# Performance work log

Measured on AMD Instinct MI355X. Metric: run time of the kernel, lower is better.

The kernel has to match this reference:

```python
import jax, jax.numpy as jnp
import numpy as np
from jax import lax

B = 1024          # batch
R = 100           # number of radical heads (TOP_RADICALS)


def _conv(x, w, b, padding):
    y = lax.conv_general_dilated(
        x, w, window_strides=(1, 1), padding=padding,
        dimension_numbers=('NCHW', 'OIHW', 'NCHW'))
    return y + b[None, :, None, None]


def _maxpool2(x):
    return lax.reduce_window(x, -jnp.inf, lax.max,
                             (1, 1, 2, 2), (1, 1, 2, 2), 'VALID')


def setup_inputs() -> dict:
    key = jax.random.key(0)
    ks = jax.random.split(key, 20)
    s = 0.05
    inp = {
        'x': jax.random.normal(ks[0], (B, 1, 98, 98), jnp.float32),
        'conv1_w': jax.random.normal(ks[1], (6, 1, 3, 3), jnp.float32) * s,
        'conv1_b': jnp.zeros((6,), jnp.float32),
        'conv2_w': jax.random.normal(ks[2], (4, 6, 6, 6), jnp.float32) * s,
        'conv2_b': jnp.zeros((4,), jnp.float32),
        'conv3_w': jax.random.normal(ks[3], (2, 4, 3, 3), jnp.float32) * s,
        'conv3_b': jnp.zeros((2,), jnp.float32),
        'fc1_w': jax.random.normal(ks[4], (200, 400), jnp.float32) * s,
        'fc1_b': jnp.zeros((400,), jnp.float32),
        'fc2_w': jax.random.normal(ks[5], (400, 200), jnp.float32) * s,
        'fc2_b': jnp.zeros((200,), jnp.float32),
        # all R per-radical heads stacked: Linear(200,140)->(140,84)->(84,42)->(42,4)
        'h1_w': jax.random.normal(ks[6], (R, 200, 140), jnp.float32) * s,
        'h1_b': jnp.zeros((R, 140), jnp.float32),
        'h2_w': jax.random.normal(ks[7], (R, 140, 84), jnp.float32) * s,
        'h2_b': jnp.zeros((R, 84), jnp.float32),
        'h3_w': jax.random.normal(ks[8], (R, 84, 42), jnp.float32) * s,
        'h3_b': jnp.zeros((R, 42), jnp.float32),
        'h4_w': jax.random.normal(ks[9], (R, 42, 4), jnp.float32) * s,
        'h4_b': jnp.zeros((R, 4), jnp.float32),
    }
    return inp


def reference(x, conv1_w, conv1_b, conv2_w, conv2_b, conv3_w, conv3_b,
              fc1_w, fc1_b, fc2_w, fc2_b,
              h1_w, h1_b, h2_w, h2_b, h3_w, h3_b, h4_w, h4_b):
    # conv trunk: conv -> relu -> maxpool, x3
    x = _maxpool2(jax.nn.relu(_conv(x, conv1_w, conv1_b, [(1, 1), (1, 1)])))  # [B,6,49,49]
    x = _maxpool2(jax.nn.relu(_conv(x, conv2_w, conv2_b, 'VALID')))           # [B,4,22,22]
    x = _maxpool2(jax.nn.relu(_conv(x, conv3_w, conv3_b, 'VALID')))           # [B,2,10,10]
    x = x.reshape(x.shape[0], -1)                                             # [B,200]
    # shared MLP trunk
    x = jax.nn.relu(x @ fc1_w + fc1_b)   # [B,400]
    x = jax.nn.relu(x @ fc2_w + fc2_b)   # [B,200]
    # R independent 4-layer heads, fused into batched einsums
    h = jax.nn.relu(jnp.einsum('bd,rdh->brh', x, h1_w) + h1_b)  # [B,R,140]
    h = jax.nn.relu(jnp.einsum('brd,rdh->brh', h, h2_w) + h2_b)  # [B,R,84]
    h = jax.nn.relu(jnp.einsum('brd,rdh->brh', h, h3_w) + h3_b)  # [B,R,42]
    h = jnp.einsum('brd,rdh->brh', h, h4_w) + h4_b               # [B,R,4]
    # torch.cat over heads along dim=1 == reshape [B, R*4]
    return h.reshape(h.shape[0], -1)
```

## Files before the change

### kernel.cpp

```cpp
#include <hip/hip_runtime.h>

#define NB 1024
#define NR 100

typedef _Float16 half_t;
typedef half_t f16x8 __attribute__((ext_vector_type(8)));
typedef float f32x4 __attribute__((ext_vector_type(4)));
typedef float f32x2 __attribute__((ext_vector_type(2)));

__device__ __forceinline__ int kmap2(int g, int j) {
    return g*4 + (j & 3) + ((j >> 2) << 4);
}

__device__ __forceinline__ f32x2 pkfma(f32x2 a, float s, f32x2 c) {
    return __builtin_elementwise_fma(a, (f32x2){s, s}, c);
}

#define GLDS(gsrc, ldst) \
    __builtin_amdgcn_global_load_lds( \
        (const __attribute__((address_space(1))) void*)(gsrc), \
        (__attribute__((address_space(3))) void*)(ldst), 16, 0, 0)

#define EOFF 2268
__global__ __launch_bounds__(256, 5) void conv12_k(const float* __restrict__ x,
        const float* __restrict__ wp1, const float* __restrict__ b1c,
        const float* __restrict__ wp2, const float* __restrict__ b2c,
        float* __restrict__ out) {
    __shared__ float img[56*56];
    __shared__ float c1p[4374];
    const int blk = blockIdx.x;
    const int b  = blk >> 2;
    const int qy = (blk >> 1) & 1, qx = blk & 1;
    const int R0 = 44*qy - 1, C0 = 44*qx - 1;
    const int tid = threadIdx.x;
    const float* xb = x + (size_t)b * 9604;

    for (int i = tid; i < 56*56; i += 256) {
        const int rr = i / 56, cc = i - rr*56;
        const int gr = R0 + rr, gc = C0 + cc;
        float v = 0.f;
        if (gr >= 0 && gr < 98 && gc >= 0 && gc < 98) v = xb[gr*98 + gc];
        img[i] = v;
    }
    __syncthreads();

    for (int pos = tid; pos < 729; pos += 256) {
        const int py = pos / 27, px = pos - py*27;
        float p[4][4];
        const float* base = img + (2*py)*56 + 2*px;
        #pragma unroll
        for (int u = 0; u < 4; ++u) {
            *(f32x2*)&p[u][0] = *(const f32x2*)(base + u*56);
            *(f32x2*)&p[u][2] = *(const f32x2*)(base + u*56 + 2);
        }
        f32x2 a2[3][4];
        #pragma unroll
        for (int g = 0; g < 3; ++g) {
            const f32x2 bv = *(const f32x2*)(b1c + g*2);
            a2[g][0] = a2[g][1] = a2[g][2] = a2[g][3] = bv;
        }
        #pragma unroll
        for (int ky = 0; ky < 3; ++ky)
            #pragma unroll
            for (int kx = 0; kx < 3; ++kx) {
                const int k = ky*3 + kx;
                const float q0 = p[ky  ][kx], q1 = p[ky  ][kx+1];
                const float q2 = p[ky+1][kx], q3 = p[ky+1][kx+1];
                #pragma unroll
                for (int g = 0; g < 3; ++g) {
                    const f32x2 wv = *(const f32x2*)(wp1 + (k*3+g)*2);
                    a2[g][0] = pkfma(wv, q0, a2[g][0]);
                    a2[g][1] = pkfma(wv, q1, a2[g][1]);
                    a2[g][2] = pkfma(wv, q2, a2[g][2]);
                    a2[g][3] = pkfma(wv, q3, a2[g][3]);
                }
            }
        const int par = px & 1, pi = px >> 1;
        #pragma unroll
        for (int g = 0; g < 3; ++g) {
            const float m0 = fmaxf(fmaxf(a2[g][0].x, a2[g][1].x),
                                   fmaxf(a2[g][2].x, a2[g][3].x));
            const float m1 = fmaxf(fmaxf(a2[g][0].y, a2[g][1].y),
                                   fmaxf(a2[g][2].y, a2[g][3].y));
            const int e0 = par ? (EOFF + ((2*g    )*27 + py)*13 + pi)
                               : (((2*g    )*27 + py)*14 + pi);
            const int e1 = par ? (EOFF + ((2*g + 1)*27 + py)*13 + pi)
                               : (((2*g + 1)*27 + py)*14 + pi);
            c1p[e0] = fmaxf(m0, 0.f);
            c1p[e1] = fmaxf(m1, 0.f);
        }
    }
    __syncthreads();

    const int wv_ = tid >> 6;
    const int ocg = __builtin_amdgcn_readfirstlane(tid >> 7);
    const int unit = ((wv_ & 1) << 6) | (tid & 63);
    if (unit >= 121) return;
    const int py = unit / 11, px = unit - py*11;
    const int y0 = 2*py;

    const float* wg = wp2 + (size_t)ocg * 432;
    f32x2 acc2[2][2];
    {
        const f32x2 bv = *(const f32x2*)(b2c + ocg*2);
        acc2[0][0] = acc2[0][1] = acc2[1][0] = acc2[1][1] = bv;
    }

    #pragma unroll
    for (int ic = 0; ic < 6; ++ic) {
        const float* pe0 = c1p + (ic*27 + y0)*14 + px;
        const float* po0 = c1p + EOFF + (ic*27 + y0)*13 + px;
        #pragma unroll
        for (int u = 0; u < 7; ++u) {
            const float* pe = pe0 + u*14;
            const float* po = po0 + u*13;
            float pr[7];
            pr[0] = pe[0]; pr[2] = pe[1]; pr[4] = pe[2]; pr[6] = pe[3];
            pr[1] = po[0]; pr[3] = po[1]; pr[5] = po[2];
            #pragma unroll
            for (int dy = 0; dy < 2; ++dy) {
                const int ky = u - dy;
                if (ky < 0 || ky > 5) continue;
                #pragma unroll
                for (int kx = 0; kx < 6; ++kx) {
                    const f32x2 wv =
                        *(const f32x2*)(wg + (ic*36 + ky*6 + kx)*2);
                    acc2[dy][0] = pkfma(wv, pr[0+kx], acc2[dy][0]);
                    acc2[dy][1] = pkfma(wv, pr[1+kx], acc2[dy][1]);
                }
            }
        }
    }

    const int PY = qy*11 + py, PX = qx*11 + px;
    {
        const float m0 = fmaxf(fmaxf(acc2[0][0].x, acc2[0][1].x),
                               fmaxf(acc2[1][0].x, acc2[1][1].x));
        const float m1 = fmaxf(fmaxf(acc2[0][0].y, acc2[0][1].y),
                               fmaxf(acc2[1][0].y, acc2[1][1].y));
        out[(((size_t)b*4 + ocg*2    )*22 + PY)*22 + PX] = fmaxf(m0, 0.f);
        out[(((size_t)b*4 + ocg*2 + 1)*22 + PY)*22 + PX] = fmaxf(m1, 0.f);
    }
}

__global__ __launch_bounds__(256) void conv3_k(const float* __restrict__ in,
        const float* __restrict__ w, const float* __restrict__ bias,
        float* __restrict__ out) {
    __shared__ float sm[1936];
    const int b = blockIdx.x;
    const int tid = threadIdx.x;
    const float* src = in + (size_t)b * 1936;
    for (int i = tid; i < 484; i += 256)
        ((float4*)sm)[i] = ((const float4*)src)[i];
    __syncthreads();
    if (tid < 200) {
        const int c = tid / 100;
        const int rem = tid % 100;
        const int py = rem / 10, px = rem % 10;
        const int y0 = 2*py, x0 = 2*px;
        float a0, a1, a2, a3;
        a0 = a1 = a2 = a3 = bias[c];
        #pragma unroll
        for (int ic = 0; ic < 4; ++ic) {
            float p[4][4];
            const float* base = sm + ic*484 + y0*22 + x0;
            #pragma unroll
            for (int u = 0; u < 4; ++u)
                #pragma unroll
                for (int v = 0; v < 4; ++v)
                    p[u][v] = base[u*22 + v];
            #pragma unroll
            for (int ky = 0; ky < 3; ++ky) {
                #pragma unroll
                for (int kx = 0; kx < 3; ++kx) {
                    const float wv = w[(c*4 + ic)*9 + ky*3 + kx];
                    a0 = fmaf(wv, p[ky  ][kx  ], a0);
                    a1 = fmaf(wv, p[ky  ][kx+1], a1);
                    a2 = fmaf(wv, p[ky+1][kx  ], a2);
                    a3 = fmaf(wv, p[ky+1][kx+1], a3);
                }
            }
        }
        float m = fmaxf(fmaxf(a0, a1), fmaxf(a2, a3));
        out[(size_t)b*200 + tid] = fmaxf(m, 0.f);
    }
}

template<bool G0OUT>
__global__ __launch_bounds__(256, 4) void gemm_k(
        const float* __restrict__ A, int lda,
        const float* __restrict__ W, const float* __restrict__ bias,
        float* __restrict__ C, int ldc,
        int M, int N, int K,
        half_t* __restrict__ g0h, half_t* __restrict__ g0l) {
    __shared__ float As[32][132];
    __shared__ float Ws[32][64];
    const int m0 = blockIdx.y * 128;
    const int n0 = blockIdx.x * 64;
    const int tid = threadIdx.x;
    const int ti = tid >> 4, tj = tid & 15;
    float acc[8][4];
    #pragma unroll
    for (int i = 0; i < 8; ++i)
        #pragma unroll
        for (int j = 0; j < 4; ++j) acc[i][j] = 0.f;

    for (int k0 = 0; k0 < K; k0 += 32) {
        #pragma unroll
        for (int i = 0; i < 4; ++i) {
            const int f = tid + i*256;
            const int m = f >> 3, kg = f & 7;
            const int kk = kg*4;
            float4 v = make_float4(0.f, 0.f, 0.f, 0.f);
            if (k0 + kk < K)
                v = *(const float4*)(A + (long)(m0 + m)*lda + k0 + kk);
            As[kk+0][m] = v.x;
            As[kk+1][m] = v.y;
            As[kk+2][m] = v.z;
            As[kk+3][m] = v.w;
        }
        #pragma unroll
        for (int i = 0; i < 2; ++i) {
            const int f = tid + i*256;
            const int kk = f >> 4, cg = f & 15;
            const int n = n0 + cg*4;
            float4 v = make_float4(0.f, 0.f, 0.f, 0.f);
            if (k0 + kk < K) {
                const float* wp = W + (long)(k0 + kk)*N;
                if (n + 3 < N) v = *(const float4*)(wp + n);
                else {
                    if (n+0 < N) v.x = wp[n+0];
                    if (n+1 < N) v.y = wp[n+1];
                    if (n+2 < N) v.z = wp[n+2];
                }
            }
            *(float4*)&Ws[kk][cg*4] = v;
        }
        __syncthreads();
        #pragma unroll
        for (int kk = 0; kk < 32; ++kk) {
            float a[8], wv[4];
            *(float4*)&a[0] = *(const float4*)&As[kk][ti*8];
            *(float4*)&a[4] = *(const float4*)&As[kk][ti*8 + 4];
            *(float4*)&wv[0] = *(const float4*)&Ws[kk][tj*4];
            #pragma unroll
            for (int i = 0; i < 8; ++i)
                #pragma unroll
                for (int j = 0; j < 4; ++j)
                    acc[i][j] = fmaf(a[i], wv[j], acc[i][j]);
        }
        __syncthreads();
    }

    const int nb = n0 + tj*4;
    float bv[4] = {0.f, 0.f, 0.f, 0.f};
    #pragma unroll
    for (int e = 0; e < 4; ++e) if (nb + e < N) bv[e] = bias[nb + e];

    if (!G0OUT) {
        #pragma unroll
        for (int i = 0; i < 8; ++i) {
            const long m = m0 + ti*8 + i;
            if (nb + 3 < N) {
                float4 v;
                v.x = fmaxf(acc[i][0] + bv[0], 0.f);
                v.y = fmaxf(acc[i][1] + bv[1], 0.f);
                v.z = fmaxf(acc[i][2] + bv[2], 0.f);
                v.w = fmaxf(acc[i][3] + bv[3], 0.f);
                *(float4*)(C + m*(long)ldc + nb) = v;
            } else {
                #pragma unroll
                for (int j = 0; j < 4; ++j)
                    if (nb + j < N)
                        C[m*(long)ldc + nb + j] = fmaxf(acc[i][j] + bv[j], 0.f);
            }
        }
    } else {
        #pragma unroll
        for (int i = 0; i < 8; ++i) {
            const int m = m0 + ti*8 + i;
            #pragma unroll
            for (int j = 0; j < 4; ++j) {
                const int k = nb + j;
                if (k < N) {
                    const float v = fmaxf(acc[i][j] + bv[j], 0.f);
                    const half_t hi = (half_t)v;
                    const half_t lo = (half_t)(v - (float)hi);
                    const int kc = k >> 5, klo = k & 31;
                    const int h = klo >> 4, rm = klo & 15;
                    const int gg = rm >> 2, rr = rm & 3;
                    const size_t idx =
                        ((size_t)((m >> 4)*7 + kc)*64 + (gg << 4) + (m & 15))*8
                        + h*4 + rr;
                    g0h[idx] = hi;
                    g0l[idx] = lo;
                }
            }
        }
    }
}

__global__ __launch_bounds__(256) void wsplit_k(
        const float* __restrict__ w1, const float* __restrict__ w2,
        const float* __restrict__ w3, const float* __restrict__ w4,
        half_t* __restrict__ f1h, half_t* __restrict__ f1l,
        half_t* __restrict__ f2h, half_t* __restrict__ f2l,
        half_t* __restrict__ f3h, half_t* __restrict__ f3l,
        half_t* __restrict__ f4h, half_t* __restrict__ f4l,
        const float* __restrict__ c1w, const float* __restrict__ c2w,
        float* __restrict__ wp1, float* __restrict__ wp2) {
    __shared__ float lds[32*140];
    const int cx = blockIdx.x, r = blockIdx.y, tid = threadIdx.x;
    if (cx == 17) {
        if (r != 0) return;
        if (tid < 27) {
            const int k = tid / 3, g = tid - (tid/3)*3;
            wp1[tid*2+0] = c1w[(g*2+0)*9 + k];
            wp1[tid*2+1] = c1w[(g*2+1)*9 + k];
        }
        for (int i = tid; i < 432; i += 256) {
            const int ocg = i / 216, k = i - ocg*216;
            wp2[i*2+0] = c2w[(ocg*2+0)*216 + k];
            wp2[i*2+1] = c2w[(ocg*2+1)*216 + k];
        }
        return;
    }
    int K, N, KC, NF, kc;
    const float* src;
    half_t *dh, *dl;
    if (cx < 7)       { K=200; N=140; KC=7; NF=9; kc=cx;    src=w1; dh=f1h; dl=f1l; }
    else if (cx < 12) { K=140; N=84;  KC=5; NF=6; kc=cx-7;  src=w2; dh=f2h; dl=f2l; }
    else if (cx < 15) { K=84;  N=42;  KC=3; NF=3; kc=cx-12; src=w3; dh=f3h; dl=f3l; }
    else              { K=42;  N=4;   KC=2; NF=1; kc=cx-15; src=w4; dh=f4h; dl=f4l; }
    const float* sb = src + (size_t)r * K * N;
    for (int i = tid; i < 32*N; i += 256) {
        const int kk = i / N, n = i - kk*N;
        const int kg = kc*32 + kk;
        lds[kk*N + n] = (kg < K) ? sb[(size_t)kg*N + n] : 0.f;
    }
    __syncthreads();
    const size_t base = ((size_t)r*KC + kc)*NF*512;
    for (int e = tid; e < NF*512; e += 256) {
        const int nf = e >> 9, rem = e & 511;
        const int l = rem >> 3, j = rem & 7;
        const int g = l >> 4, c = l & 15;
        const int kl = kmap2(g, j);
        const int n = nf*16 + c;
        const float v = (n < N) ? lds[kl*N + n] : 0.f;
        const half_t hi = (half_t)v;
        const half_t lo = (half_t)(v - (float)hi);
        dh[base + (size_t)nf*512 + rem] = hi;
        dl[base + (size_t)nf*512 + rem] = lo;
    }
}

#define MFMA(a, b, c) __builtin_amdgcn_mfma_f32_16x16x32_f16(a, b, c, 0, 0, 0)

__global__ __launch_bounds__(256, 2) void head_k(
        const half_t* __restrict__ g0h, const half_t* __restrict__ g0l,
        const half_t* __restrict__ w1h, const half_t* __restrict__ w1l,
        const half_t* __restrict__ w2h, const half_t* __restrict__ w2l,
        const half_t* __restrict__ w3h, const half_t* __restrict__ w3l,
        const half_t* __restrict__ w4h, const half_t* __restrict__ w4l,
        const float* __restrict__ b1, const float* __restrict__ b2,
        const float* __restrict__ b3, const float* __restrict__ b4,
        float* __restrict__ out) {
    constexpr int CH = 18*512;
    __shared__ half_t wb[2*CH];
    __shared__ float bl[270];
    const int bid = blockIdx.x;
    const int cx  = bid & 7;
    const int kb  = bid >> 3;
    const int r   = ((kb >> 3) << 3) + cx;
    if (r >= NR) return;
    const int mt  = kb & 7;
    const int tid = threadIdx.x;
    if (tid < 140) bl[tid]       = b1[(size_t)r*140 + tid];
    if (tid < 84)  bl[140 + tid] = b2[(size_t)r*84  + tid];
    if (tid < 42)  bl[224 + tid] = b3[(size_t)r*42  + tid];
    if (tid < 4)   bl[266 + tid] = b4[(size_t)r*4   + tid];
    const int w = tid >> 6, l = tid & 63;
    const int g4 = ((l >> 4) & 3) * 4;
    const int mb0 = mt*8 + w*2;
    const size_t loff = (size_t)l * 8;

    auto stage1 = [&](int kc, half_t* buf) {
        const half_t* hs = w1h + ((size_t)r*7 + kc)*9*512;
        const half_t* ls = w1l + ((size_t)r*7 + kc)*9*512;
        #pragma unroll
        for (int p0 = 0; p0 < 3; ++p0) {
            const int p = w + p0*4;
            if (p < 9) {
                GLDS(hs + (size_t)p*512 + loff, buf + p*512);
                GLDS(ls + (size_t)p*512 + loff, buf + (9+p)*512);
            }
        }
    };
    auto stage2 = [&](int kc, half_t* buf) {
        const half_t* hs = w2h + ((size_t)r*5 + kc)*6*512;
        const half_t* ls = w2l + ((size_t)r*5 + kc)*6*512;
        #pragma unroll
        for (int p0 = 0; p0 < 2; ++p0) {
            const int p = w + p0*4;
            if (p < 6) {
                GLDS(hs + (size_t)p*512 + loff, buf + p*512);
                GLDS(ls + (size_t)p*512 + loff, buf + (6+p)*512);
            }
        }
    };
    auto stage3 = [&](int kc, half_t* buf) {
        const half_t* hs = w3h + ((size_t)r*3 + kc)*3*512;
        const half_t* ls = w3l + ((size_t)r*3 + kc)*3*512;
        if (w < 3) {
            GLDS(hs + (size_t)w*512 + loff, buf + w*512);
            GLDS(ls + (size_t)w*512 + loff, buf + (3+w)*512);
        }
    };

    f16x8 bhv[2][2], blv[2][2];
    stage1(0, wb);
    #pragma unroll
    for (int mb = 0; mb < 2; ++mb) {
        const size_t bo = ((size_t)(mb0 + mb)*7 + 0)*512 + loff;
        bhv[0][mb] = *(const f16x8*)(g0h + bo);
        blv[0][mb] = *(const f16x8*)(g0l + bo);
    }
    __syncthreads();
    f32x4 a1[2][9] = {};
    #pragma unroll
    for (int kc = 0; kc < 7; ++kc) {
        const half_t* cur = wb + (kc & 1)*CH;
        if (kc < 6) {
            stage1(kc+1, wb + ((kc+1) & 1)*CH);
            #pragma unroll
            for (int mb = 0; mb < 2; ++mb) {
                const size_t bo = ((size_t)(mb0 + mb)*7 + kc + 1)*512 + loff;
                bhv[(kc+1)&1][mb] = *(const f16x8*)(g0h + bo);
                blv[(kc+1)&1][mb] = *(const f16x8*)(g0l + bo);
            }
        } else {
            stage2(0, wb + CH);
        }
        #pragma unroll
        for (int nf = 0; nf < 9; ++nf) {
            const f16x8 wh = *(const f16x8*)(cur + nf*512 + loff);
            const f16x8 wl = *(const f16x8*)(cur + (9+nf)*512 + loff);
            #pragma unroll
            for (int mb = 0; mb < 2; ++mb) {
                a1[mb][nf] = MFMA(wh, bhv[kc&1][mb], a1[mb][nf]);
                a1[mb][nf] = MFMA(wh, blv[kc&1][mb], a1[mb][nf]);
                a1[mb][nf] = MFMA(wl, bhv[kc&1][mb], a1[mb][nf]);
            }
        }
        __syncthreads();
    }
    f16x8 b2h[2][5], b2l[2][5];
    #pragma unroll
    for (int kc = 0; kc < 5; ++kc)
        #pragma unroll
        for (int h = 0; h < 2; ++h) {
            const int nf = kc*2 + h;
            #pragma unroll
            for (int mb = 0; mb < 2; ++mb)
                #pragma unroll
                for (int rr = 0; rr < 4; ++rr) {
                    float v = 0.f;
                    if (nf < 9) {
                        const int n = nf*16 + g4 + rr;
                        v = (n < 140) ? fmaxf(a1[mb][nf][rr] + bl[n], 0.f) : 0.f;
                    }
                    const half_t hi = (half_t)v;
                    const half_t lo = (half_t)(v - (float)hi);
                    b2h[mb][kc][h*4+rr] = hi;
                    b2l[mb][kc][h*4+rr] = lo;
                }
        }
    f32x4 a2[2][6] = {};
    #pragma unroll
    for (int kc = 0; kc < 5; ++kc) {
        const half_t* cur = wb + (((kc+1) & 1))*CH;
        if (kc < 4) stage2(kc+1, wb + (kc & 1)*CH);
        else        stage3(0,    wb + (kc & 1)*CH);
        #pragma unroll
        for (int nf = 0; nf < 6; ++nf) {
            const f16x8 wh = *(const f16x8*)(cur + nf*512 + loff);
            const f16x8 wl = *(const f16x8*)(cur + (6+nf)*512 + loff);
            #pragma unroll
            for (int mb = 0; mb < 2; ++mb) {
                a2[mb][nf] = MFMA(wh, b2h[mb][kc], a2[mb][nf]);
                a2[mb][nf] = MFMA(wh, b2l[mb][kc], a2[mb][nf]);
                a2[mb][nf] = MFMA(wl, b2h[mb][kc], a2[mb][nf]);
            }
        }
        __syncthreads();
    }
    f16x8 b3h[2][3], b3l[2][3];
    #pragma unroll
    for (int kc = 0; kc < 3; ++kc)
        #pragma unroll
        for (int h = 0; h < 2; ++h) {
            const int nf = kc*2 + h;
            #pragma unroll
            for (int mb = 0; mb < 2; ++mb)
                #pragma unroll
                for (int rr = 0; rr < 4; ++rr) {
                    float v = 0.f;
                    if (nf < 6) {
                        const int n = nf*16 + g4 + rr;
                        v = (n < 84) ? fmaxf(a2[mb][nf][rr] + bl[140 + n], 0.f) : 0.f;
                    }
                    const half_t hi = (half_t)v;
                    const half_t lo = (half_t)(v - (float)hi);
                    b3h[mb][kc][h*4+rr] = hi;
                    b3l[mb][kc][h*4+rr] = lo;
                }
        }
    f32x4 a3[2][3] = {};
    #pragma unroll
    for (int kc = 0; kc < 3; ++kc) {
        const half_t* cur = wb + (kc & 1)*CH;
        if (kc < 2) stage3(kc+1, wb + ((kc+1) & 1)*CH);
        #pragma unroll
        for (int nf = 0; nf < 3; ++nf) {
            const f16x8 wh = *(const f16x8*)(cur + nf*512 + loff);
            const f16x8 wl = *(const f16x8*)(cur + (3+nf)*512 + loff);
            #pragma unroll
            for (int mb = 0; mb < 2; ++mb) {
                a3[mb][nf] = MFMA(wh, b3h[mb][kc], a3[mb][nf]);
                a3[mb][nf] = MFMA(wh, b3l[mb][kc], a3[mb][nf]);
                a3[mb][nf] = MFMA(wl, b3h[mb][kc], a3[mb][nf]);
            }
        }
        __syncthreads();
    }
    f16x8 b4h[2][2], b4l[2][2];
    #pragma unroll
    for (int kc = 0; kc < 2; ++kc)
        #pragma unroll
        for (int h = 0; h < 2; ++h) {
            const int nf = kc*2 + h;
            #pragma unroll
            for (int mb = 0; mb < 2; ++mb)
                #pragma unroll
                for (int rr = 0; rr < 4; ++rr) {
                    float v = 0.f;
                    if (nf < 3) {
                        const int n = nf*16 + g4 + rr;
                        v = (n < 42) ? fmaxf(a3[mb][nf][rr] + bl[224 + n], 0.f) : 0.f;
                    }
                    const half_t hi = (half_t)v;
                    const half_t lo = (half_t)(v - (float)hi);
                    b4h[mb][kc][h*4+rr] = hi;
                    b4l[mb][kc][h*4+rr] = lo;
                }
        }
    f32x4 a4[2] = {};
    #pragma unroll
    for (int kc = 0; kc < 2; ++kc) {
        const size_t wo = ((size_t)r*2 + kc)*512 + loff;
        const f16x8 wh = *(const f16x8*)(w4h + wo);
        const f16x8 wl = *(const f16x8*)(w4l + wo);
        #pragma unroll
        for (int mb = 0; mb < 2; ++mb) {
            a4[mb] = MFMA(wh, b4h[mb][kc], a4[mb]);
            a4[mb] = MFMA(wh, b4l[mb][kc], a4[mb]);
            a4[mb] = MFMA(wl, b4h[mb][kc], a4[mb]);
        }
    }
    if ((l >> 4) == 0) {
        #pragma unroll
        for (int mb = 0; mb < 2; ++mb) {
            const int b = (mb0 + mb)*16 + (l & 15);
            float4 o;
            o.x = a4[mb][0] + bl[266];
            o.y = a4[mb][1] + bl[267];
            o.z = a4[mb][2] + bl[268];
            o.w = a4[mb][3] + bl[269];
            *(float4*)(out + (size_t)b*400 + r*4) = o;
        }
    }
}

extern "C" void kernel_launch(void* const* d_in, const int* in_sizes, int n_in,
                              void* d_out, int out_size, void* d_ws, size_t ws_size,
                              hipStream_t stream) {
    const float* x    = (const float*)d_in[0];
    const float* c1w  = (const float*)d_in[1];
    const float* c1b  = (const float*)d_in[2];
    const float* c2w  = (const float*)d_in[3];
    const float* c2b  = (const float*)d_in[4];
    const float* c3w  = (const float*)d_in[5];
    const float* c3b  = (const float*)d_in[6];
    const float* fc1w = (const float*)d_in[7];
    const float* fc1b = (const float*)d_in[8];
    const float* fc2w = (const float*)d_in[9];
    const float* fc2b = (const float*)d_in[10];
    const float* h1w  = (const float*)d_in[11];
    const float* h1b  = (const float*)d_in[12];
    const float* h2w  = (const float*)d_in[13];
    const float* h2b  = (const float*)d_in[14];
    const float* h3w  = (const float*)d_in[15];
    const float* h3b  = (const float*)d_in[16];
    const float* h4w  = (const float*)d_in[17];
    const float* h4b  = (const float*)d_in[18];
    float* out = (float*)d_out;

    char* ws = (char*)d_ws;
    size_t o = 0;
    float* t2 = (float*)(ws + o); o += (size_t)NB*4*484*4;
    float* t3 = (float*)(ws + o); o += (size_t)NB*200*4;
    float* f1 = (float*)(ws + o); o += (size_t)NB*400*4;
    half_t* g0h = (half_t*)(ws + o); o += (size_t)64*7*512*2;
    half_t* g0l = (half_t*)(ws + o); o += (size_t)64*7*512*2;
    half_t* w1h = (half_t*)(ws + o); o += (size_t)NR*7*9*512*2;
    half_t* w1l = (half_t*)(ws + o); o += (size_t)NR*7*9*512*2;
    half_t* w2h = (half_t*)(ws + o); o += (size_t)NR*5*6*512*2;
    half_t* w2l = (half_t*)(ws + o); o += (size_t)NR*5*6*512*2;
    half_t* w3h = (half_t*)(ws + o); o += (size_t)NR*3*3*512*2;
    half_t* w3l = (half_t*)(ws + o); o += (size_t)NR*3*3*512*2;
    half_t* w4h = (half_t*)(ws + o); o += (size_t)NR*2*1*512*2;
    half_t* w4l = (half_t*)(ws + o); o += (size_t)NR*2*1*512*2;
    float* wp1 = (float*)(ws + o); o += 64*4;
    float* wp2 = (float*)(ws + o); o += 896*4;

    hipMemsetAsync(g0h, 0, (size_t)64*7*512*2*2, stream);

    wsplit_k<<<dim3(18, NR), 256, 0, stream>>>(h1w, h2w, h3w, h4w,
        w1h, w1l, w2h, w2l, w3h, w3l, w4h, w4l, c1w, c2w, wp1, wp2);

    conv12_k<<<NB*4, 256, 0, stream>>>(x, wp1, c1b, wp2, c2b, t2);
    conv3_k<<<NB, 256, 0, stream>>>(t2, c3w, c3b, t3);

    gemm_k<false><<<dim3(7, 8), 256, 0, stream>>>(
        t3, 200, fc1w, fc1b, f1, 400, NB, 400, 200, nullptr, nullptr);
    gemm_k<true><<<dim3(4, 8), 256, 0, stream>>>(
        f1, 400, fc2w, fc2b, nullptr, 0, NB, 200, 400, g0h, g0l);

    head_k<<<832, 256, 0, stream>>>(
        g0h, g0l, w1h, w1l, w2h, w2l, w3h, w3l, w4h, w4l,
        h1b, h2b, h3b, h4b, out);

    (void)in_sizes; (void)n_in; (void)out_size; (void)ws_size;
}
```

Baseline: 195.1 us.

## Split conv2 input channels across waves, de-interleave image LDS, fuse weight split into fc2

In conv12, the conv2 stage now splits input channels between the two wave pairs, and each thread computes both output-channel pairs. Partial sums are reduced through shared memory, which lets all four waves do useful work instead of idling half the threads' output-channel split. The input image tile is stored in even/odd column planes to avoid strided or misaligned LDS reads. The head-weight fp16 split kernel is merged into the fc2 GEMM launch as extra blocks, and the memset is removed by having fc2 write zero padding up to 224. Conv weight packing moves to a tiny separate kernel. Together these cut launch count and overlap the weight preprocessing with the small fc2 GEMM.

```diff
diff --git a/kernel.cpp b/kernel.cpp
--- a/kernel.cpp
+++ b/kernel.cpp
@@ -21,12 +21,29 @@
         (const __attribute__((address_space(1))) void*)(gsrc), \
         (__attribute__((address_space(3))) void*)(ldst), 16, 0, 0)
 
+__global__ __launch_bounds__(256) void wpack_k(
+        const float* __restrict__ c1w, const float* __restrict__ c2w,
+        float* __restrict__ wp1, float* __restrict__ wp2) {
+    const int t = threadIdx.x;
+    if (t < 27) {
+        const int k = t / 3, g = t - (t/3)*3;
+        wp1[t*2+0] = c1w[(g*2+0)*9 + k];
+        wp1[t*2+1] = c1w[(g*2+1)*9 + k];
+    }
+    for (int i = t; i < 432; i += 256) {
+        const int ocg = i / 216, k = i - ocg*216;
+        wp2[i*2+0] = c2w[(ocg*2+0)*216 + k];
+        wp2[i*2+1] = c2w[(ocg*2+1)*216 + k];
+    }
+}
+
 #define EOFF 2268
+#define IO   1568
 __global__ __launch_bounds__(256, 5) void conv12_k(const float* __restrict__ x,
         const float* __restrict__ wp1, const float* __restrict__ b1c,
         const float* __restrict__ wp2, const float* __restrict__ b2c,
         float* __restrict__ out) {
-    __shared__ float img[56*56];
+    __shared__ float img[3136];
     __shared__ float c1p[4374];
     const int blk = blockIdx.x;
     const int b  = blk >> 2;
@@ -35,23 +52,25 @@
     const int tid = threadIdx.x;
     const float* xb = x + (size_t)b * 9604;
 
-    for (int i = tid; i < 56*56; i += 256) {
+    for (int i = tid; i < 3136; i += 256) {
         const int rr = i / 56, cc = i - rr*56;
         const int gr = R0 + rr, gc = C0 + cc;
         float v = 0.f;
         if (gr >= 0 && gr < 98 && gc >= 0 && gc < 98) v = xb[gr*98 + gc];
-        img[i] = v;
+        img[((cc & 1) ? IO : 0) + rr*28 + (cc >> 1)] = v;
     }
     __syncthreads();
 
     for (int pos = tid; pos < 729; pos += 256) {
         const int py = pos / 27, px = pos - py*27;
         float p[4][4];
-        const float* base = img + (2*py)*56 + 2*px;
         #pragma unroll
         for (int u = 0; u < 4; ++u) {
-            *(f32x2*)&p[u][0] = *(const f32x2*)(base + u*56);
-            *(f32x2*)&p[u][2] = *(const f32x2*)(base + u*56 + 2);
+            const int ro = (2*py + u)*28;
+            p[u][0] = img[ro + px];
+            p[u][2] = img[ro + px + 1];
+            p[u][1] = img[IO + ro + px];
+            p[u][3] = img[IO + ro + px + 1];
         }
         f32x2 a2[3][4];
         #pragma unroll
@@ -93,53 +112,82 @@
     __syncthreads();
 
     const int wv_ = tid >> 6;
-    const int ocg = __builtin_amdgcn_readfirstlane(tid >> 7);
+    const int ich = __builtin_amdgcn_readfirstlane(tid >> 7);
     const int unit = ((wv_ & 1) << 6) | (tid & 63);
-    if (unit >= 121) return;
-    const int py = unit / 11, px = unit - py*11;
+    const bool act = unit < 121;
+    const int py = act ? unit / 11 : 0;
+    const int px = act ? unit - py*11 : 0;
     const int y0 = 2*py;
 
-    const float* wg = wp2 + (size_t)ocg * 432;
-    f32x2 acc2[2][2];
-    {
-        const f32x2 bv = *(const f32x2*)(b2c + ocg*2);
-        acc2[0][0] = acc2[0][1] = acc2[1][0] = acc2[1][1] = bv;
-    }
-
-    #pragma unroll
-    for (int ic = 0; ic < 6; ++ic) {
-        const float* pe0 = c1p + (ic*27 + y0)*14 + px;
-        const float* po0 = c1p + EOFF + (ic*27 + y0)*13 + px;
-        #pragma unroll
-        for (int u = 0; u < 7; ++u) {
-            const float* pe = pe0 + u*14;
-            const float* po = po0 + u*13;
-            float pr[7];
-            pr[0] = pe[0]; pr[2] = pe[1]; pr[4] = pe[2]; pr[6] = pe[3];
-            pr[1] = po[0]; pr[3] = po[1]; pr[5] = po[2];
-            #pragma unroll
-            for (int dy = 0; dy < 2; ++dy) {
-                const int ky = u - dy;
-                if (ky < 0 || ky > 5) continue;
-                #pragma unroll
-                for (int kx = 0; kx < 6; ++kx) {
-                    const f32x2 wv =
-                        *(const f32x2*)(wg + (ic*36 + ky*6 + kx)*2);
-                    acc2[dy][0] = pkfma(wv, pr[0+kx], acc2[dy][0]);
-                    acc2[dy][1] = pkfma(wv, pr[1+kx], acc2[dy][1]);
-                }
-            }
-        }
-    }
-
-    const int PY = qy*11 + py, PX = qx*11 + px;
-    {
-        const float m0 = fmaxf(fmaxf(acc2[0][0].x, acc2[0][1].x),
-                               fmaxf(acc2[1][0].x, acc2[1][1].x));
-        const float m1 = fmaxf(fmaxf(acc2[0][0].y, acc2[0][1].y),
-                               fmaxf(acc2[1][0].y, acc2[1][1].y));
-        out[(((size_t)b*4 + ocg*2    )*22 + PY)*22 + PX] = fmaxf(m0, 0.f);
-        out[(((size_t)b*4 + ocg*2 + 1)*22 + PY)*22 + PX] = fmaxf(m1, 0.f);
+    f32x2 acc[2][2][2] = {};
+    if (act) {
+        #pragma unroll
+        for (int ic3 = 0; ic3 < 3; ++ic3) {
+            const int ic = ich*3 + ic3;
+            const float* pe0 = c1p + (ic*27 + y0)*14 + px;
+            const float* po0 = c1p + EOFF + (ic*27 + y0)*13 + px;
+            #pragma unroll
+            for (int u = 0; u < 7; ++u) {
+                const float* pe = pe0 + u*14;
+                const float* po = po0 + u*13;
+                float pr[7];
+                pr[0] = pe[0]; pr[2] = pe[1]; pr[4] = pe[2]; pr[6] = pe[3];
+                pr[1] = po[0]; pr[3] = po[1]; pr[5] = po[2];
+                #pragma unroll
+                for (int dy = 0; dy < 2; ++dy) {
+                    const int ky = u - dy;
+                    if (ky < 0 || ky > 5) continue;
+                    #pragma unroll
+                    for (int kx = 0; kx < 6; ++kx) {
+                        const f32x2 w0 =
+                            *(const f32x2*)(wp2 + (ic*36 + ky*6 + kx)*2);
+                        const f32x2 w1 =
+                            *(const f32x2*)(wp2 + 432 + (ic*36 + ky*6 + kx)*2);
+                        acc[0][dy][0] = pkfma(w0, pr[0+kx], acc[0][dy][0]);
+                        acc[0][dy][1] = pkfma(w0, pr[1+kx], acc[0][dy][1]);
+                        acc[1][dy][0] = pkfma(w1, pr[0+kx], acc[1][dy][0]);
+                        acc[1][dy][1] = pkfma(w1, pr[1+kx], acc[1][dy][1]);
+                    }
+                }
+            }
+        }
+    }
+    float* pbuf = img;
+    if (act && ich == 1) {
+        #pragma unroll
+        for (int p = 0; p < 2; ++p)
+            #pragma unroll
+            for (int dy = 0; dy < 2; ++dy)
+                #pragma unroll
+                for (int dx = 0; dx < 2; ++dx) {
+                    const int j = ((p*2 + dy)*2 + dx)*2;
+                    pbuf[(j    )*128 + unit] = acc[p][dy][dx].x;
+                    pbuf[(j + 1)*128 + unit] = acc[p][dy][dx].y;
+                }
+    }
+    __syncthreads();
+    if (act && ich == 0) {
+        #pragma unroll
+        for (int p = 0; p < 2; ++p)
+            #pragma unroll
+            for (int dy = 0; dy < 2; ++dy)
+                #pragma unroll
+                for (int dx = 0; dx < 2; ++dx) {
+                    const int j = ((p*2 + dy)*2 + dx)*2;
+                    acc[p][dy][dx].x += pbuf[(j    )*128 + unit];
+                    acc[p][dy][dx].y += pbuf[(j + 1)*128 + unit];
+                }
+        const int PY = qy*11 + py, PX = qx*11 + px;
+        #pragma unroll
+        for (int p = 0; p < 2; ++p) {
+            const f32x2 bv = *(const f32x2*)(b2c + p*2);
+            const float m0 = fmaxf(fmaxf(acc[p][0][0].x, acc[p][0][1].x),
+                                   fmaxf(acc[p][1][0].x, acc[p][1][1].x)) + bv.x;
+            const float m1 = fmaxf(fmaxf(acc[p][0][0].y, acc[p][0][1].y),
+                                   fmaxf(acc[p][1][0].y, acc[p][1][1].y)) + bv.y;
+            out[(((size_t)b*4 + p*2    )*22 + PY)*22 + PX] = fmaxf(m0, 0.f);
+            out[(((size_t)b*4 + p*2 + 1)*22 + PY)*22 + PX] = fmaxf(m1, 0.f);
+        }
     }
 }
 
@@ -187,16 +235,16 @@
 }
 
 template<bool G0OUT>
-__global__ __launch_bounds__(256, 4) void gemm_k(
+__device__ __forceinline__ void gemm_body(float* pool, int bx, int by,
         const float* __restrict__ A, int lda,
         const float* __restrict__ W, const float* __restrict__ bias,
         float* __restrict__ C, int ldc,
         int M, int N, int K,
         half_t* __restrict__ g0h, half_t* __restrict__ g0l) {
-    __shared__ float As[32][132];
-    __shared__ float Ws[32][64];
-    const int m0 = blockIdx.y * 128;
-    const int n0 = blockIdx.x * 64;
+    float (*As)[132] = (float(*)[132])pool;
+    float* Ws = pool + 32*132;
+    const int m0 = by * 128;
+    const int n0 = bx * 64;
     const int tid = threadIdx.x;
     const int ti = tid >> 4, tj = tid & 15;
     float acc[8][4];
@@ -234,7 +282,7 @@
                     if (n+2 < N) v.z = wp[n+2];
                 }
             }
-            *(float4*)&Ws[kk][cg*4] = v;
+            *(float4*)&Ws[kk*64 + cg*4] = v;
         }
         __syncthreads();
         #pragma unroll
@@ -242,7 +290,7 @@
             float a[8], wv[4];
             *(float4*)&a[0] = *(const float4*)&As[kk][ti*8];
             *(float4*)&a[4] = *(const float4*)&As[kk][ti*8 + 4];
-            *(float4*)&wv[0] = *(const float4*)&Ws[kk][tj*4];
+            *(float4*)&wv[0] = *(const float4*)&Ws[kk*64 + tj*4];
             #pragma unroll
             for (int i = 0; i < 8; ++i)
                 #pragma unroll
@@ -282,8 +330,9 @@
             #pragma unroll
             for (int j = 0; j < 4; ++j) {
                 const int k = nb + j;
-                if (k < N) {
-                    const float v = fmaxf(acc[i][j] + bv[j], 0.f);
+                if (k < 224) {
+                    float v = 0.f;
+                    if (k < N) v = fmaxf(acc[i][j] + bv[j], 0.f);
                     const half_t hi = (half_t)v;
                     const half_t lo = (half_t)(v - (float)hi);
                     const int kc = k >> 5, klo = k & 31;
@@ -300,31 +349,35 @@
     }
 }
 
-__global__ __launch_bounds__(256) void wsplit_k(
+__global__ __launch_bounds__(256, 4) void fc1_k(
+        const float* __restrict__ A, const float* __restrict__ W,
+        const float* __restrict__ bias, float* __restrict__ C) {
+    __shared__ float pool[32*132 + 32*64];
+    gemm_body<false>(pool, blockIdx.x, blockIdx.y, A, 200, W, bias, C, 400,
+                     NB, 400, 200, nullptr, nullptr);
+}
+
+__global__ __launch_bounds__(256, 4) void fc2ws_k(
+        const float* __restrict__ A, const float* __restrict__ W,
+        const float* __restrict__ bias,
+        half_t* __restrict__ g0h, half_t* __restrict__ g0l,
         const float* __restrict__ w1, const float* __restrict__ w2,
         const float* __restrict__ w3, const float* __restrict__ w4,
         half_t* __restrict__ f1h, half_t* __restrict__ f1l,
         half_t* __restrict__ f2h, half_t* __restrict__ f2l,
         half_t* __restrict__ f3h, half_t* __restrict__ f3l,
-        half_t* __restrict__ f4h, half_t* __restrict__ f4l,
-        const float* __restrict__ c1w, const float* __restrict__ c2w,
-        float* __restrict__ wp1, float* __restrict__ wp2) {
-    __shared__ float lds[32*140];
-    const int cx = blockIdx.x, r = blockIdx.y, tid = threadIdx.x;
-    if (cx == 17) {
-        if (r != 0) return;
-        if (tid < 27) {
-            const int k = tid / 3, g = tid - (tid/3)*3;
-            wp1[tid*2+0] = c1w[(g*2+0)*9 + k];
-            wp1[tid*2+1] = c1w[(g*2+1)*9 + k];
-        }
-        for (int i = tid; i < 432; i += 256) {
-            const int ocg = i / 216, k = i - ocg*216;
-            wp2[i*2+0] = c2w[(ocg*2+0)*216 + k];
-            wp2[i*2+1] = c2w[(ocg*2+1)*216 + k];
-        }
+        half_t* __restrict__ f4h, half_t* __restrict__ f4l) {
+    __shared__ float pool[32*132 + 32*64];
+    const int bid = blockIdx.x;
+    const int tid = threadIdx.x;
+    if (bid < 32) {
+        gemm_body<true>(pool, bid & 3, bid >> 2, A, 400, W, bias,
+                        nullptr, 0, NB, 200, 400, g0h, g0l);
         return;
     }
+    const int w = bid - 32;
+    const int cx = w % 17, r = w / 17;
+    float* lds = pool;
     int K, N, KC, NF, kc;
     const float* src;
     half_t *dh, *dl;
@@ -623,19 +676,12 @@
     float* wp1 = (float*)(ws + o); o += 64*4;
     float* wp2 = (float*)(ws + o); o += 896*4;
 
-    hipMemsetAsync(g0h, 0, (size_t)64*7*512*2*2, stream);
-
-    wsplit_k<<<dim3(18, NR), 256, 0, stream>>>(h1w, h2w, h3w, h4w,
-        w1h, w1l, w2h, w2l, w3h, w3l, w4h, w4l, c1w, c2w, wp1, wp2);
-
+    wpack_k<<<1, 256, 0, stream>>>(c1w, c2w, wp1, wp2);
     conv12_k<<<NB*4, 256, 0, stream>>>(x, wp1, c1b, wp2, c2b, t2);
     conv3_k<<<NB, 256, 0, stream>>>(t2, c3w, c3b, t3);
-
-    gemm_k<false><<<dim3(7, 8), 256, 0, stream>>>(
-        t3, 200, fc1w, fc1b, f1, 400, NB, 400, 200, nullptr, nullptr);
-    gemm_k<true><<<dim3(4, 8), 256, 0, stream>>>(
-        f1, 400, fc2w, fc2b, nullptr, 0, NB, 200, 400, g0h, g0l);
-
+    fc1_k<<<dim3(7, 8), 256, 0, stream>>>(t3, fc1w, fc1b, f1);
+    fc2ws_k<<<32 + 1700, 256, 0, stream>>>(f1, fc2w, fc2b, g0h, g0l,
+        h1w, h2w, h3w, h4w, w1h, w1l, w2h, w2l, w3h, w3l, w4h, w4l);
     head_k<<<832, 256, 0, stream>>>(
         g0h, g0l, w1h, w1l, w2h, w2l, w3h, w3l, w4h, w4l,
         h1b, h2b, h3b, h4b, out);
```

Result: faster. 184.3 us (-5.5%).
